# Performance work log

Measured on AMD Instinct MI355X. Metric: run time of the kernel, lower is better.

Reference implementation:

```python
import jax, jax.numpy as jnp
import numpy as np

THETA = 10000.0
NUM_HEADS = 16


def apply_rope(x, pos, theta):
    # x: [..., s, d_k] with d_k even; pos: [s] (broadcasts over leading dims)
    d_k = x.shape[-1]
    inv_freq = 1.0 / (theta ** (jnp.arange(0, d_k, 2, dtype=x.dtype) / d_k))  # [d_k/2]
    ang = pos.astype(x.dtype)[..., None] * inv_freq  # [s, d_k/2]
    cos, sin = jnp.cos(ang), jnp.sin(ang)
    xr = x.reshape(x.shape[:-1] + (d_k // 2, 2))
    x0, x1 = xr[..., 0], xr[..., 1]
    out0 = x0 * cos - x1 * sin
    out1 = x0 * sin + x1 * cos
    return jnp.stack((out0, out1), axis=-1).reshape(x.shape)


def setup_inputs() -> dict:
    key = jax.random.key(0)
    ks = jax.random.split(key, 5)
    B, S, D = 4, 2048, 1024
    sigma = 2.0 / (D + D) ** 0.5
    return {
        "x": jax.random.normal(ks[0], (B, S, D), dtype=jnp.float32),
        "token_positions": jnp.arange(S, dtype=jnp.int64 if jax.config.jax_enable_x64 else jnp.int32),
        "wq": jax.random.normal(ks[1], (D, D), dtype=jnp.float32) * sigma,
        "wk": jax.random.normal(ks[2], (D, D), dtype=jnp.float32) * sigma,
        "wv": jax.random.normal(ks[3], (D, D), dtype=jnp.float32) * sigma,
        "wo": jax.random.normal(ks[4], (D, D), dtype=jnp.float32) * sigma,
    }


def reference(x, token_positions, wq, wk, wv, wo):
    B, S, D = x.shape
    H = NUM_HEADS
    d_k = D // H

    def proj(w, t):  # weight [out, in], t [..., in]
        return jnp.einsum('oi,bsi->bso', w, t)

    def heads(t):  # [b, s, (h d)] -> [b, h, s, d]
        return t.reshape(B, S, H, d_k).transpose(0, 2, 1, 3)

    Q = heads(proj(wq, x))
    K = heads(proj(wk, x))
    V = heads(proj(wv, x))
    Q = apply_rope(Q, token_positions, THETA)
    K = apply_rope(K, token_positions, THETA)

    scores = jnp.einsum('bhqd,bhkd->bhqk', Q, K) * (d_k ** -0.5)
    causal = jnp.tril(jnp.ones((S, S), dtype=bool))
    scores = jnp.where(causal, scores, -jnp.inf)
    attn = jax.nn.softmax(scores.astype(jnp.float32), axis=-1).astype(scores.dtype)
    out = jnp.einsum('bhqk,bhkd->bhqd', attn, V)
    out = out.transpose(0, 2, 1, 3).reshape(B, S, D)
    return jnp.einsum('oi,bsi->bso', wo, out)
```

## Files before the change

### kernel.cpp

```cpp
#include <hip/hip_runtime.h>
#include <cstdint>
#include <cstddef>

#define Bv 4
#define Sv 2048
#define Hv 16
#define Dv 1024
#define Mv (Bv*Sv)

typedef __attribute__((ext_vector_type(8))) short short8;
typedef __attribute__((ext_vector_type(8))) unsigned short ushort8v;
typedef __attribute__((ext_vector_type(4))) float f32x4;

__device__ inline float bf2f(unsigned short u) {
  union { unsigned int i; float f; } x; x.i = ((unsigned int)u) << 16; return x.f;
}
__device__ inline unsigned short f2bf(float f) {
  union { float f; unsigned int i; } x; x.f = f;
  unsigned int r = x.i + 0x7FFFu + ((x.i >> 16) & 1u);
  return (unsigned short)(r >> 16);
}

typedef __attribute__((address_space(1))) const unsigned short gu16;
typedef __attribute__((address_space(3))) unsigned short lu16;
__device__ inline void gld_lds16(const unsigned short* g, unsigned short* l) {
  __builtin_amdgcn_global_load_lds((gu16*)g, (lu16*)l, 16, 0, 0);
}

__global__ __launch_bounds__(256) void cvt_f32_bf16(const float* __restrict__ src,
                                                    unsigned short* __restrict__ dst, int n4) {
  int i = blockIdx.x * 256 + threadIdx.x;
  if (i >= n4) return;
  float4 v = reinterpret_cast<const float4*>(src)[i];
  ushort4 o;
  o.x = f2bf(v.x); o.y = f2bf(v.y); o.z = f2bf(v.z); o.w = f2bf(v.w);
  reinterpret_cast<ushort4*>(dst)[i] = o;
}

__global__ __launch_bounds__(256) void cvt3_f32_bf16(const float* __restrict__ s0,
                                                     const float* __restrict__ s1,
                                                     const float* __restrict__ s2,
                                                     unsigned short* __restrict__ dst) {
  int i = blockIdx.x * 256 + threadIdx.x;
  int w = i >> 18, off = i & 262143;
  const float* src = (w == 0) ? s0 : (w == 1) ? s1 : s2;
  float4 v = reinterpret_cast<const float4*>(src)[off];
  ushort4 o;
  o.x = f2bf(v.x); o.y = f2bf(v.y); o.z = f2bf(v.z); o.w = f2bf(v.w);
  reinterpret_cast<ushort4*>(dst)[i] = o;
}

__global__ __launch_bounds__(256) void rope_table_k(const int* __restrict__ pos,
                                                    float* __restrict__ tab) {
  int idx = blockIdx.x * 256 + threadIdx.x;
  int s = idx >> 5, i = idx & 31;
  float p = (float)pos[s];
  float a = p * __builtin_exp2f(-0.41524101186092027f * (float)i);
  tab[(s << 6) + i]      = __builtin_cosf(a);
  tab[(s << 6) + 32 + i] = __builtin_sinf(a);
}

__device__ __forceinline__ void xcd_swizzle(int& bm, int& bn) {
  const int nx = gridDim.x;
  const int nwg = nx * gridDim.y;
  int flat = blockIdx.y * nx + blockIdx.x;
  if ((nwg & 7) == 0) {
    int q = nwg >> 3;
    flat = (flat & 7) * q + (flat >> 3);
  }
  bm = (flat / nx) * 128;
  bn = (flat % nx) * 128;
}

__device__ inline void storeC(float* p, float v) { *p = v; }
__device__ inline void storeC(unsigned short* p, float v) { *p = f2bf(v); }

template <typename CT>
__global__ __launch_bounds__(256) void gemm_bt_128(
    const unsigned short* __restrict__ A,
    const unsigned short* __restrict__ B,
    CT* __restrict__ C,
    int M, int N, int K) {
  __shared__ unsigned short As[128 * 32];
  __shared__ unsigned short Bs[128 * 32];
  const int tid = threadIdx.x;
  const int wave = tid >> 6, lane = tid & 63;
  int bm, bn;
  xcd_swizzle(bm, bn);
  const int wr = (wave >> 1) * 64, wc = (wave & 1) * 64;

  f32x4 acc[4][4] = {};

  const int c0 = wave * 2, c1 = c0 + 1;
  const int sr0 = c0 * 16 + (lane >> 2);
  const int sr1 = c1 * 16 + (lane >> 2);
  const int scol = (lane & 3) * 8;

  const unsigned short* gA0 = A + (size_t)(bm + sr0) * K + scol;
  const unsigned short* gA1 = A + (size_t)(bm + sr1) * K + scol;
  const unsigned short* gB0 = B + (size_t)(bn + sr0) * K + scol;
  const unsigned short* gB1 = B + (size_t)(bn + sr1) * K + scol;
  unsigned short* lA0 = &As[c0 * 512];
  unsigned short* lA1 = &As[c1 * 512];
  unsigned short* lB0 = &Bs[c0 * 512];
  unsigned short* lB1 = &Bs[c1 * 512];

  const int fr = lane & 15;
  const int fk = (lane >> 4) * 8;

  for (int k0 = 0; k0 < K; k0 += 32) {
    gld_lds16(gA0 + k0, lA0);
    gld_lds16(gA1 + k0, lA1);
    gld_lds16(gB0 + k0, lB0);
    gld_lds16(gB1 + k0, lB1);
    __syncthreads();
    short8 af[4], bfr[4];
#pragma unroll
    for (int m = 0; m < 4; m++)
      af[m] = *reinterpret_cast<const short8*>(&As[(wr + m * 16 + fr) * 32 + fk]);
#pragma unroll
    for (int n = 0; n < 4; n++)
      bfr[n] = *reinterpret_cast<const short8*>(&Bs[(wc + n * 16 + fr) * 32 + fk]);
#pragma unroll
    for (int m = 0; m < 4; m++)
#pragma unroll
      for (int n = 0; n < 4; n++)
        acc[m][n] = __builtin_amdgcn_mfma_f32_16x16x32_bf16(af[m], bfr[n], acc[m][n], 0, 0, 0);
    __syncthreads();
  }

  const int er = (lane >> 4) * 4, ec = lane & 15;
#pragma unroll
  for (int m = 0; m < 4; m++)
#pragma unroll
    for (int n = 0; n < 4; n++)
#pragma unroll
      for (int r = 0; r < 4; r++) {
        int row = bm + wr + m * 16 + er + r;
        int col = bn + wc + n * 16 + ec;
        storeC(&C[(size_t)row * N + col], acc[m][n][r]);
      }
}

__global__ __launch_bounds__(256) void gemm_qkv(
    const unsigned short* __restrict__ A,
    const unsigned short* __restrict__ B,
    unsigned short* __restrict__ Qp,
    unsigned short* __restrict__ Kp,
    unsigned short* __restrict__ Vt,
    const float* __restrict__ tab) {
  const int K = Dv;
  __shared__ unsigned short As[128 * 32];
  __shared__ unsigned short Bs[128 * 32];
  const int tid = threadIdx.x;
  const int wave = tid >> 6, lane = tid & 63;
  int bm, bn;
  xcd_swizzle(bm, bn);
  const int wr = (wave >> 1) * 64, wc = (wave & 1) * 64;

  f32x4 acc[4][4] = {};

  const int c0 = wave * 2, c1 = c0 + 1;
  const int sr0 = c0 * 16 + (lane >> 2);
  const int sr1 = c1 * 16 + (lane >> 2);
  const int scol = (lane & 3) * 8;

  const unsigned short* gA0 = A + (size_t)(bm + sr0) * K + scol;
  const unsigned short* gA1 = A + (size_t)(bm + sr1) * K + scol;
  const unsigned short* gB0 = B + (size_t)(bn + sr0) * K + scol;
  const unsigned short* gB1 = B + (size_t)(bn + sr1) * K + scol;
  unsigned short* lA0 = &As[c0 * 512];
  unsigned short* lA1 = &As[c1 * 512];
  unsigned short* lB0 = &Bs[c0 * 512];
  unsigned short* lB1 = &Bs[c1 * 512];

  const int fr = lane & 15;
  const int fk = (lane >> 4) * 8;

  for (int k0 = 0; k0 < K; k0 += 32) {
    gld_lds16(gA0 + k0, lA0);
    gld_lds16(gA1 + k0, lA1);
    gld_lds16(gB0 + k0, lB0);
    gld_lds16(gB1 + k0, lB1);
    __syncthreads();
    short8 af[4], bfr[4];
#pragma unroll
    for (int m = 0; m < 4; m++)
      af[m] = *reinterpret_cast<const short8*>(&As[(wr + m * 16 + fr) * 32 + fk]);
#pragma unroll
    for (int n = 0; n < 4; n++)
      bfr[n] = *reinterpret_cast<const short8*>(&Bs[(wc + n * 16 + fr) * 32 + fk]);
#pragma unroll
    for (int m = 0; m < 4; m++)
#pragma unroll
      for (int n = 0; n < 4; n++)
        acc[m][n] = __builtin_amdgcn_mfma_f32_16x16x32_bf16(af[m], bfr[n], acc[m][n], 0, 0, 0);
    __syncthreads();
  }

  const int er = (lane >> 4) * 4, ec = lane & 15;
  const int region = bn >> 10;
  if (region < 2) {
    unsigned short* T = (region == 0) ? Qp : Kp;
#pragma unroll
    for (int m = 0; m < 4; m++)
#pragma unroll
      for (int n = 0; n < 4; n++) {
        const int col = bn + wc + n * 16 + ec;
        const int ccol = col & (Dv - 1);
        const int ii = (ccol & 63) >> 1;
        const bool odd = col & 1;
#pragma unroll
        for (int r = 0; r < 4; r++) {
          int row = bm + wr + m * 16 + er + r;
          int s = row & (Sv - 1);
          float v = acc[m][n][r];
          float pv = __shfl_xor(v, 1);
          float cc = tab[(s << 6) + ii];
          float sn = tab[(s << 6) + 32 + ii];
          float o = odd ? __builtin_fmaf(pv, sn, v * cc)
                        : __builtin_fmaf(v, cc, -(pv * sn));
          T[(size_t)row * Dv + ccol] = f2bf(o);
        }
      }
  } else {
#pragma unroll
    for (int m = 0; m < 4; m++)
#pragma unroll
      for (int n = 0; n < 4; n++) {
        const int dfull = (bn - 2048) + wc + n * 16 + ec;
        const int row0 = bm + wr + m * 16 + er;
        const int bb = row0 >> 11, s = row0 & (Sv - 1);
        const size_t vtrow = ((size_t)bb * 16 + (dfull >> 6)) * 64 + (dfull & 63);
        ushort4 ov;
        ov.x = f2bf(acc[m][n][0]);
        ov.y = f2bf(acc[m][n][1]);
        ov.z = f2bf(acc[m][n][2]);
        ov.w = f2bf(acc[m][n][3]);
        *reinterpret_cast<ushort4*>(Vt + vtrow * Sv + s) = ov;
      }
  }
}

__device__ __forceinline__ void softmax_strip(
    f32x4 (&sacc)[2][4], const bool lastt, const int qrel0,
    float (&mrun2)[2], float (&lrun)[2], f32x4 (&oacc)[2][4],
    unsigned int (&pk)[2][4][2]) {
  const float c1 = 0.18033688011112042f;
#pragma unroll
  for (int qf = 0; qf < 2; ++qf) {
    const int qrel = qrel0 + qf * 16;
    float pv[4][4];
    float mx = -INFINITY;
#pragma unroll
    for (int kf = 0; kf < 4; ++kf)
#pragma unroll
      for (int r = 0; r < 4; ++r) {
        float s = sacc[qf][kf][r];
        if (lastt) s = (kf * 16 + r > qrel) ? -INFINITY : s;
        pv[kf][r] = s;
        mx = fmaxf(mx, s);
      }
    mx = fmaxf(mx, __shfl_xor(mx, 16));
    mx = fmaxf(mx, __shfl_xor(mx, 32));
    float pm = mx * c1;
    if (__any(pm > mrun2[qf] + 8.0f)) {
      float m2 = fmaxf(mrun2[qf], pm);
      float sfq = __builtin_exp2f(mrun2[qf] - m2);
      lrun[qf] *= sfq;
#pragma unroll
      for (int dc = 0; dc < 4; ++dc)
#pragma unroll
        for (int r = 0; r < 4; ++r) oacc[qf][dc][r] *= sfq;
      mrun2[qf] = m2;
    }
    const float nm = -mrun2[qf];
    float ps = 0.f;
#pragma unroll
    for (int kf = 0; kf < 4; ++kf)
#pragma unroll
      for (int r = 0; r < 4; ++r) {
        float p = __builtin_exp2f(__builtin_fmaf(pv[kf][r], c1, nm));
        ps += p;
        pv[kf][r] = p;
      }
    ps += __shfl_xor(ps, 16);
    ps += __shfl_xor(ps, 32);
    lrun[qf] += ps;
#pragma unroll
    for (int kf = 0; kf < 4; ++kf)
#pragma unroll
      for (int hh = 0; hh < 2; ++hh) {
        unsigned int rr;
        asm("v_cvt_pk_bf16_f32 %0, %1, %2"
            : "=v"(rr) : "v"(pv[kf][2 * hh]), "v"(pv[kf][2 * hh + 1]));
        pk[qf][kf][hh] = rr;
      }
  }
}

__device__ __forceinline__ void pv_strip(
    const short8 (&vfr)[2][4], const unsigned int (&pk)[2][4][2],
    f32x4 (&oacc)[2][4], const int idx0, const int idx1, const bool hi) {
#pragma unroll
  for (int ks = 0; ks < 2; ++ks)
#pragma unroll
    for (int qf = 0; qf < 2; ++qf) {
      int ra = __builtin_amdgcn_ds_bpermute(idx0, (int)pk[qf][2 * ks][0]);
      int rb = __builtin_amdgcn_ds_bpermute(idx0, (int)pk[qf][2 * ks + 1][0]);
      int rc = __builtin_amdgcn_ds_bpermute(idx0, (int)pk[qf][2 * ks][1]);
      int rd = __builtin_amdgcn_ds_bpermute(idx0, (int)pk[qf][2 * ks + 1][1]);
      int re = __builtin_amdgcn_ds_bpermute(idx1, (int)pk[qf][2 * ks][0]);
      int rf = __builtin_amdgcn_ds_bpermute(idx1, (int)pk[qf][2 * ks + 1][0]);
      int rg = __builtin_amdgcn_ds_bpermute(idx1, (int)pk[qf][2 * ks][1]);
      int rh = __builtin_amdgcn_ds_bpermute(idx1, (int)pk[qf][2 * ks + 1][1]);
      union { unsigned int u[4]; short8 v; } pw;
      pw.u[0] = hi ? (unsigned)rb : (unsigned)ra;
      pw.u[1] = hi ? (unsigned)rd : (unsigned)rc;
      pw.u[2] = hi ? (unsigned)rf : (unsigned)re;
      pw.u[3] = hi ? (unsigned)rh : (unsigned)rg;
      __builtin_amdgcn_s_setprio(1);
#pragma unroll
      for (int dc = 0; dc < 4; ++dc)
        oacc[qf][dc] = __builtin_amdgcn_mfma_f32_16x16x32_bf16(vfr[ks][dc], pw.v, oacc[qf][dc], 0, 0, 0);
      __builtin_amdgcn_s_setprio(0);
    }
}

__global__ __launch_bounds__(256, 2) void attn_mfma(
    const unsigned short* __restrict__ Q,
    const unsigned short* __restrict__ K,
    const unsigned short* __restrict__ Vt,
    unsigned short* __restrict__ O) {
  __shared__ __align__(16) unsigned short ldsK[2][4096];
  __shared__ __align__(16) unsigned short ldsV[2][4096];
  const int tid = threadIdx.x;
  const int wave = tid >> 6, lane = tid & 63;
  const int g = lane >> 4, m = lane & 15;
  const int F = blockIdx.x;
  const int q7 = F >> 3;
  const int bh = ((F & 7) << 3) | (q7 & 7);
  const int bi = q7 >> 3;
  const int b = bh >> 4, h = bh & 15;
  const int j = bi * 4 + wave;
  const int sA = j, sB = 63 - j;
  const int qA0 = sA * 32, qB0 = sB * 32;
  const int ntA = (sA >> 1) + 1, ntB = (sB >> 1) + 1;
  const int ntBmax = ((63 - bi * 4) >> 1) + 1;
  const size_t qkbase = ((size_t)b * Sv) * Dv + (size_t)h * 64;
  const size_t vtbase = (size_t)bh * 64 * Sv;
  const f32x4 zf = {0.f, 0.f, 0.f, 0.f};

  int srowS[2], scolS[2];
#pragma unroll
  for (int i = 0; i < 2; ++i) {
    int s = ((i * 4 + wave) << 6) + lane;
    int s2 = s ^ ((s >> 3) & 7);
    srowS[i] = s2 >> 3;
    scolS[i] = (s2 & 7) * 8;
  }

  short8 qA[2][2], qB[2][2];
#pragma unroll
  for (int qf = 0; qf < 2; ++qf)
#pragma unroll
    for (int ks = 0; ks < 2; ++ks) {
      qA[qf][ks] = *reinterpret_cast<const short8*>(
          Q + qkbase + (size_t)(qA0 + qf * 16 + m) * Dv + ks * 32 + g * 8);
      qB[qf][ks] = *reinterpret_cast<const short8*>(
          Q + qkbase + (size_t)(qB0 + qf * 16 + m) * Dv + ks * 32 + g * 8);
    }

  int offL[2][4];
#pragma unroll
  for (int ks = 0; ks < 2; ++ks)
#pragma unroll
    for (int f = 0; f < 4; ++f)
      offL[ks][f] = (f * 16 + m) * 64 + ((((ks << 2) + g) ^ (m & 7)) * 8);

  f32x4 oA[2][4] = {}, oB[2][4] = {};
  float mA[2] = {-INFINITY, -INFINITY}, mB[2] = {-INFINITY, -INFINITY};
  float lA[2] = {0.f, 0.f}, lB[2] = {0.f, 0.f};

  const int idx0 = (((g & 1) << 5) + m) << 2;
  const int idx1 = idx0 + 64;
  const bool hi = (g >= 2);
  int qrelA = qA0 + m - 4 * g;
  int qrelB = qB0 + m - 4 * g;

  auto STAGE = [&](int c, int t) {
    const int kb = t << 6;
#pragma unroll
    for (int i = 0; i < 2; ++i) {
      gld_lds16(K + qkbase + (size_t)(kb + srowS[i]) * Dv + scolS[i],
                &ldsK[c][(i * 4 + wave) * 512]);
      gld_lds16(Vt + vtbase + (size_t)srowS[i] * Sv + kb + scolS[i],
                &ldsV[c][(i * 4 + wave) * 512]);
    }
  };

  STAGE(0, 0);
  __syncthreads();
  int cur = 0;

  for (int t = 0; t < ntBmax; ++t) {
    if (t + 1 < ntBmax) STAGE(cur ^ 1, t + 1);

    if (t < ntB) {
      const bool actA = (t < ntA);
      f32x4 sAacc[2][4], sBacc[2][4];
      short8 kfr[4];
#pragma unroll
      for (int kf = 0; kf < 4; ++kf)
        kfr[kf] = *reinterpret_cast<const short8*>(&ldsK[cur][offL[0][kf]]);
      __builtin_amdgcn_s_setprio(1);
#pragma unroll
      for (int qf = 0; qf < 2; ++qf)
#pragma unroll
        for (int kf = 0; kf < 4; ++kf)
          sBacc[qf][kf] = __builtin_amdgcn_mfma_f32_16x16x32_bf16(kfr[kf], qB[qf][0], zf, 0, 0, 0);
      if (actA)
#pragma unroll
        for (int qf = 0; qf < 2; ++qf)
#pragma unroll
          for (int kf = 0; kf < 4; ++kf)
            sAacc[qf][kf] = __builtin_amdgcn_mfma_f32_16x16x32_bf16(kfr[kf], qA[qf][0], zf, 0, 0, 0);
      __builtin_amdgcn_s_setprio(0);
#pragma unroll
      for (int kf = 0; kf < 4; ++kf)
        kfr[kf] = *reinterpret_cast<const short8*>(&ldsK[cur][offL[1][kf]]);
      __builtin_amdgcn_s_setprio(1);
#pragma unroll
      for (int qf = 0; qf < 2; ++qf)
#pragma unroll
        for (int kf = 0; kf < 4; ++kf)
          sBacc[qf][kf] = __builtin_amdgcn_mfma_f32_16x16x32_bf16(kfr[kf], qB[qf][1], sBacc[qf][kf], 0, 0, 0);
      if (actA)
#pragma unroll
        for (int qf = 0; qf < 2; ++qf)
#pragma unroll
          for (int kf = 0; kf < 4; ++kf)
            sAacc[qf][kf] = __builtin_amdgcn_mfma_f32_16x16x32_bf16(kfr[kf], qA[qf][1], sAacc[qf][kf], 0, 0, 0);
      __builtin_amdgcn_s_setprio(0);

      short8 vfr[2][4];
#pragma unroll
      for (int ks = 0; ks < 2; ++ks)
#pragma unroll
        for (int dc = 0; dc < 4; ++dc)
          vfr[ks][dc] = *reinterpret_cast<const short8*>(&ldsV[cur][offL[ks][dc]]);

      unsigned int pkB[2][4][2], pkA[2][4][2];
      softmax_strip(sBacc, t == ntB - 1, qrelB, mB, lB, oB, pkB);
      if (actA) softmax_strip(sAacc, t == ntA - 1, qrelA, mA, lA, oA, pkA);
      pv_strip(vfr, pkB, oB, idx0, idx1, hi);
      if (actA) pv_strip(vfr, pkA, oA, idx0, idx1, hi);

      qrelA -= 64; qrelB -= 64;
    }

    __syncthreads();
    cur ^= 1;
  }

#pragma unroll
  for (int qf = 0; qf < 2; ++qf) {
    float rnA = 1.0f / lA[qf];
    float rnB = 1.0f / lB[qf];
    size_t rowA = (size_t)(qA0 + qf * 16 + m);
    size_t rowB = (size_t)(qB0 + qf * 16 + m);
#pragma unroll
    for (int dc = 0; dc < 4; ++dc) {
      ushort4 ov;
      ov.x = f2bf(oA[qf][dc][0] * rnA);
      ov.y = f2bf(oA[qf][dc][1] * rnA);
      ov.z = f2bf(oA[qf][dc][2] * rnA);
      ov.w = f2bf(oA[qf][dc][3] * rnA);
      *reinterpret_cast<ushort4*>(O + qkbase + rowA * Dv + dc * 16 + 4 * g) = ov;
      ov.x = f2bf(oB[qf][dc][0] * rnB);
      ov.y = f2bf(oB[qf][dc][1] * rnB);
      ov.z = f2bf(oB[qf][dc][2] * rnB);
      ov.w = f2bf(oB[qf][dc][3] * rnB);
      *reinterpret_cast<ushort4*>(O + qkbase + rowB * Dv + dc * 16 + 4 * g) = ov;
    }
  }
}

extern "C" void kernel_launch(void* const* d_in, const int* in_sizes, int n_in,
                              void* d_out, int out_size, void* d_ws, size_t ws_size,
                              hipStream_t stream) {
  const float* x   = (const float*)d_in[0];
  const int*   pos = (const int*)d_in[1];
  const float* wq  = (const float*)d_in[2];
  const float* wk  = (const float*)d_in[3];
  const float* wv  = (const float*)d_in[4];
  const float* wo  = (const float*)d_in[5];
  float* out = (float*)d_out;

  char* w = (char*)d_ws;
  unsigned short* xb    = (unsigned short*)(w);
  unsigned short* wqkvb = (unsigned short*)(w + (16u << 20));
  unsigned short* wob   = (unsigned short*)(w + (22u << 20));
  unsigned short* Qp    = (unsigned short*)(w + (24u << 20));
  unsigned short* Kp    = (unsigned short*)(w + (40u << 20));
  unsigned short* Vt    = (unsigned short*)(w + (56u << 20));
  float*          tab   = (float*)(w + (72u << 20));

  rope_table_k<<<(Sv * 32) / 256, 256, 0, stream>>>(pos, tab);
  cvt_f32_bf16<<<(Mv * Dv / 4) / 256, 256, 0, stream>>>(x, xb, Mv * Dv / 4);
  cvt3_f32_bf16<<<(3 * Dv * Dv / 4) / 256, 256, 0, stream>>>(wq, wk, wv, wqkvb);
  cvt_f32_bf16<<<(Dv * Dv / 4) / 256, 256, 0, stream>>>(wo, wob, Dv * Dv / 4);

  gemm_qkv<<<dim3(3 * Dv / 128, Mv / 128), 256, 0, stream>>>(xb, wqkvb, Qp, Kp, Vt, tab);

  attn_mfma<<<512, 256, 0, stream>>>(Qp, Kp, Vt, xb);

  gemm_bt_128<float><<<dim3(Dv / 128, Mv / 128), 256, 0, stream>>>(xb, wob, out, Mv, Dv, Dv);
}
```

Measured before the change: 225.2 us.

## Split attention KV range across wave pairs and merge partial softmax via LDS

Each block now handles two query strip pairs, and each pair is processed by two waves that each cover half of the key range. The waves combine their partial max, sum and output through LDS with a log-sum-exp merge. K and V fragments are now read directly from global memory instead of being staged through double-buffered LDS, and the grid doubles to 1024 blocks. The goal is more parallelism and shorter per-wave serial chains. The cost is that shared K/V reuse across waves is lost, fragment loads become uncoalesced global reads, and a merge step is added.

```diff
diff --git a/kernel.cpp b/kernel.cpp
--- a/kernel.cpp
+++ b/kernel.cpp
@@ -332,33 +332,27 @@
     const unsigned short* __restrict__ K,
     const unsigned short* __restrict__ Vt,
     unsigned short* __restrict__ O) {
-  __shared__ __align__(16) unsigned short ldsK[2][4096];
-  __shared__ __align__(16) unsigned short ldsV[2][4096];
+  __shared__ float cbO[2][64][32];
+  __shared__ float cbML[2][64][4];
   const int tid = threadIdx.x;
   const int wave = tid >> 6, lane = tid & 63;
   const int g = lane >> 4, m = lane & 15;
   const int F = blockIdx.x;
-  const int q7 = F >> 3;
-  const int bh = ((F & 7) << 3) | (q7 & 7);
-  const int bi = q7 >> 3;
-  const int b = bh >> 4, h = bh & 15;
-  const int j = bi * 4 + wave;
+  const int i6 = F >> 3;
+  const int bh = ((F & 7) << 3) | (i6 & 7);
+  const int gidx = i6 >> 3;
+  const int pi = wave >> 1, half = wave & 1;
+  const int j = gidx * 2 + pi;
   const int sA = j, sB = 63 - j;
   const int qA0 = sA * 32, qB0 = sB * 32;
   const int ntA = (sA >> 1) + 1, ntB = (sB >> 1) + 1;
-  const int ntBmax = ((63 - bi * 4) >> 1) + 1;
+  const int T0 = (ntB + 1) >> 1;
+  const int tBeg = half ? T0 : 0;
+  const int tEnd = half ? ntB : T0;
+  const int b = bh >> 4, h = bh & 15;
   const size_t qkbase = ((size_t)b * Sv) * Dv + (size_t)h * 64;
   const size_t vtbase = (size_t)bh * 64 * Sv;
   const f32x4 zf = {0.f, 0.f, 0.f, 0.f};
-
-  int srowS[2], scolS[2];
-#pragma unroll
-  for (int i = 0; i < 2; ++i) {
-    int s = ((i * 4 + wave) << 6) + lane;
-    int s2 = s ^ ((s >> 3) & 7);
-    srowS[i] = s2 >> 3;
-    scolS[i] = (s2 & 7) * 8;
-  }
 
   short8 qA[2][2], qB[2][2];
 #pragma unroll
@@ -371,12 +365,14 @@
           Q + qkbase + (size_t)(qB0 + qf * 16 + m) * Dv + ks * 32 + g * 8);
     }
 
-  int offL[2][4];
-#pragma unroll
-  for (int ks = 0; ks < 2; ++ks)
-#pragma unroll
-    for (int f = 0; f < 4; ++f)
-      offL[ks][f] = (f * 16 + m) * 64 + ((((ks << 2) + g) ^ (m & 7)) * 8);
+  const unsigned short* kp[4];
+  const unsigned short* vp[4];
+#pragma unroll
+  for (int kf = 0; kf < 4; ++kf)
+    kp[kf] = K + qkbase + (size_t)(kf * 16 + m) * Dv + g * 8 + (size_t)tBeg * 64 * Dv;
+#pragma unroll
+  for (int dc = 0; dc < 4; ++dc)
+    vp[dc] = Vt + vtbase + (size_t)(dc * 16 + m) * Sv + g * 8 + tBeg * 64;
 
   f32x4 oA[2][4] = {}, oB[2][4] = {};
   float mA[2] = {-INFINITY, -INFINITY}, mB[2] = {-INFINITY, -INFINITY};
@@ -385,103 +381,143 @@
   const int idx0 = (((g & 1) << 5) + m) << 2;
   const int idx1 = idx0 + 64;
   const bool hi = (g >= 2);
-  int qrelA = qA0 + m - 4 * g;
-  int qrelB = qB0 + m - 4 * g;
-
-  auto STAGE = [&](int c, int t) {
-    const int kb = t << 6;
-#pragma unroll
-    for (int i = 0; i < 2; ++i) {
-      gld_lds16(K + qkbase + (size_t)(kb + srowS[i]) * Dv + scolS[i],
-                &ldsK[c][(i * 4 + wave) * 512]);
-      gld_lds16(Vt + vtbase + (size_t)srowS[i] * Sv + kb + scolS[i],
-                &ldsV[c][(i * 4 + wave) * 512]);
-    }
-  };
-
-  STAGE(0, 0);
+  int qrelA = qA0 + m - 4 * g - tBeg * 64;
+  int qrelB = qB0 + m - 4 * g - tBeg * 64;
+
+  for (int t = tBeg; t < tEnd; ++t) {
+    const bool actA = (t < ntA);
+    f32x4 sAacc[2][4], sBacc[2][4];
+    short8 kfr[4];
+#pragma unroll
+    for (int kf = 0; kf < 4; ++kf)
+      kfr[kf] = *reinterpret_cast<const short8*>(kp[kf]);
+    __builtin_amdgcn_s_setprio(1);
+#pragma unroll
+    for (int qf = 0; qf < 2; ++qf)
+#pragma unroll
+      for (int kf = 0; kf < 4; ++kf)
+        sBacc[qf][kf] = __builtin_amdgcn_mfma_f32_16x16x32_bf16(kfr[kf], qB[qf][0], zf, 0, 0, 0);
+    if (actA)
+#pragma unroll
+      for (int qf = 0; qf < 2; ++qf)
+#pragma unroll
+        for (int kf = 0; kf < 4; ++kf)
+          sAacc[qf][kf] = __builtin_amdgcn_mfma_f32_16x16x32_bf16(kfr[kf], qA[qf][0], zf, 0, 0, 0);
+    __builtin_amdgcn_s_setprio(0);
+#pragma unroll
+    for (int kf = 0; kf < 4; ++kf)
+      kfr[kf] = *reinterpret_cast<const short8*>(kp[kf] + 32);
+    __builtin_amdgcn_s_setprio(1);
+#pragma unroll
+    for (int qf = 0; qf < 2; ++qf)
+#pragma unroll
+      for (int kf = 0; kf < 4; ++kf)
+        sBacc[qf][kf] = __builtin_amdgcn_mfma_f32_16x16x32_bf16(kfr[kf], qB[qf][1], sBacc[qf][kf], 0, 0, 0);
+    if (actA)
+#pragma unroll
+      for (int qf = 0; qf < 2; ++qf)
+#pragma unroll
+        for (int kf = 0; kf < 4; ++kf)
+          sAacc[qf][kf] = __builtin_amdgcn_mfma_f32_16x16x32_bf16(kfr[kf], qA[qf][1], sAacc[qf][kf], 0, 0, 0);
+    __builtin_amdgcn_s_setprio(0);
+
+    short8 vfr[2][4];
+#pragma unroll
+    for (int ks = 0; ks < 2; ++ks)
+#pragma unroll
+      for (int dc = 0; dc < 4; ++dc)
+        vfr[ks][dc] = *reinterpret_cast<const short8*>(vp[dc] + ks * 32);
+
+    unsigned int pkB[2][4][2], pkA[2][4][2];
+    softmax_strip(sBacc, t == ntB - 1, qrelB, mB, lB, oB, pkB);
+    if (actA) softmax_strip(sAacc, t == ntA - 1, qrelA, mA, lA, oA, pkA);
+    pv_strip(vfr, pkB, oB, idx0, idx1, hi);
+    if (actA) pv_strip(vfr, pkA, oA, idx0, idx1, hi);
+
+#pragma unroll
+    for (int kf = 0; kf < 4; ++kf) kp[kf] += (size_t)64 * Dv;
+#pragma unroll
+    for (int dc = 0; dc < 4; ++dc) vp[dc] += 64;
+    qrelA -= 64; qrelB -= 64;
+  }
+
+  if (half) {
+#pragma unroll
+    for (int qf = 0; qf < 2; ++qf) {
+      cbML[pi][lane][qf * 2]     = mB[qf];
+      cbML[pi][lane][qf * 2 + 1] = lB[qf];
+#pragma unroll
+      for (int dc = 0; dc < 4; ++dc)
+#pragma unroll
+        for (int r = 0; r < 4; ++r)
+          cbO[pi][lane][qf * 16 + dc * 4 + r] = oB[qf][dc][r];
+    }
+  }
   __syncthreads();
-  int cur = 0;
-
-  for (int t = 0; t < ntBmax; ++t) {
-    if (t + 1 < ntBmax) STAGE(cur ^ 1, t + 1);
-
-    if (t < ntB) {
-      const bool actA = (t < ntA);
-      f32x4 sAacc[2][4], sBacc[2][4];
-      short8 kfr[4];
-#pragma unroll
-      for (int kf = 0; kf < 4; ++kf)
-        kfr[kf] = *reinterpret_cast<const short8*>(&ldsK[cur][offL[0][kf]]);
-      __builtin_amdgcn_s_setprio(1);
-#pragma unroll
-      for (int qf = 0; qf < 2; ++qf)
-#pragma unroll
-        for (int kf = 0; kf < 4; ++kf)
-          sBacc[qf][kf] = __builtin_amdgcn_mfma_f32_16x16x32_bf16(kfr[kf], qB[qf][0], zf, 0, 0, 0);
-      if (actA)
-#pragma unroll
-        for (int qf = 0; qf < 2; ++qf)
-#pragma unroll
-          for (int kf = 0; kf < 4; ++kf)
-            sAacc[qf][kf] = __builtin_amdgcn_mfma_f32_16x16x32_bf16(kfr[kf], qA[qf][0], zf, 0, 0, 0);
-      __builtin_amdgcn_s_setprio(0);
-#pragma unroll
-      for (int kf = 0; kf < 4; ++kf)
-        kfr[kf] = *reinterpret_cast<const short8*>(&ldsK[cur][offL[1][kf]]);
-      __builtin_amdgcn_s_setprio(1);
-#pragma unroll
-      for (int qf = 0; qf < 2; ++qf)
-#pragma unroll
-        for (int kf = 0; kf < 4; ++kf)
-          sBacc[qf][kf] = __builtin_amdgcn_mfma_f32_16x16x32_bf16(kfr[kf], qB[qf][1], sBacc[qf][kf], 0, 0, 0);
-      if (actA)
-#pragma unroll
-        for (int qf = 0; qf < 2; ++qf)
-#pragma unroll
-          for (int kf = 0; kf < 4; ++kf)
-            sAacc[qf][kf] = __builtin_amdgcn_mfma_f32_16x16x32_bf16(kfr[kf], qA[qf][1], sAacc[qf][kf], 0, 0, 0);
-      __builtin_amdgcn_s_setprio(0);
-
-      short8 vfr[2][4];
-#pragma unroll
-      for (int ks = 0; ks < 2; ++ks)
-#pragma unroll
-        for (int dc = 0; dc < 4; ++dc)
-          vfr[ks][dc] = *reinterpret_cast<const short8*>(&ldsV[cur][offL[ks][dc]]);
-
-      unsigned int pkB[2][4][2], pkA[2][4][2];
-      softmax_strip(sBacc, t == ntB - 1, qrelB, mB, lB, oB, pkB);
-      if (actA) softmax_strip(sAacc, t == ntA - 1, qrelA, mA, lA, oA, pkA);
-      pv_strip(vfr, pkB, oB, idx0, idx1, hi);
-      if (actA) pv_strip(vfr, pkA, oA, idx0, idx1, hi);
-
-      qrelA -= 64; qrelB -= 64;
-    }
-
-    __syncthreads();
-    cur ^= 1;
-  }
-
-#pragma unroll
-  for (int qf = 0; qf < 2; ++qf) {
-    float rnA = 1.0f / lA[qf];
-    float rnB = 1.0f / lB[qf];
-    size_t rowA = (size_t)(qA0 + qf * 16 + m);
-    size_t rowB = (size_t)(qB0 + qf * 16 + m);
-#pragma unroll
-    for (int dc = 0; dc < 4; ++dc) {
-      ushort4 ov;
-      ov.x = f2bf(oA[qf][dc][0] * rnA);
-      ov.y = f2bf(oA[qf][dc][1] * rnA);
-      ov.z = f2bf(oA[qf][dc][2] * rnA);
-      ov.w = f2bf(oA[qf][dc][3] * rnA);
-      *reinterpret_cast<ushort4*>(O + qkbase + rowA * Dv + dc * 16 + 4 * g) = ov;
-      ov.x = f2bf(oB[qf][dc][0] * rnB);
-      ov.y = f2bf(oB[qf][dc][1] * rnB);
-      ov.z = f2bf(oB[qf][dc][2] * rnB);
-      ov.w = f2bf(oB[qf][dc][3] * rnB);
-      *reinterpret_cast<ushort4*>(O + qkbase + rowB * Dv + dc * 16 + 4 * g) = ov;
+  if (!half) {
+#pragma unroll
+    for (int qf = 0; qf < 2; ++qf) {
+      float mH = cbML[pi][lane][qf * 2], lH = cbML[pi][lane][qf * 2 + 1];
+      float m2 = fmaxf(mB[qf], mH);
+      float sfL = __builtin_exp2f(mB[qf] - m2);
+      float sfH = __builtin_exp2f(mH - m2);
+      lB[qf] = lB[qf] * sfL + lH * sfH;
+#pragma unroll
+      for (int dc = 0; dc < 4; ++dc)
+#pragma unroll
+        for (int r = 0; r < 4; ++r)
+          oB[qf][dc][r] = oB[qf][dc][r] * sfL + cbO[pi][lane][qf * 16 + dc * 4 + r] * sfH;
+    }
+  }
+  __syncthreads();
+  if (half) {
+#pragma unroll
+    for (int qf = 0; qf < 2; ++qf) {
+      cbML[pi][lane][qf * 2]     = mA[qf];
+      cbML[pi][lane][qf * 2 + 1] = lA[qf];
+#pragma unroll
+      for (int dc = 0; dc < 4; ++dc)
+#pragma unroll
+        for (int r = 0; r < 4; ++r)
+          cbO[pi][lane][qf * 16 + dc * 4 + r] = oA[qf][dc][r];
+    }
+  }
+  __syncthreads();
+  if (!half) {
+#pragma unroll
+    for (int qf = 0; qf < 2; ++qf) {
+      float mH = cbML[pi][lane][qf * 2], lH = cbML[pi][lane][qf * 2 + 1];
+      float m2 = fmaxf(mA[qf], mH);
+      float sfL = __builtin_exp2f(mA[qf] - m2);
+      float sfH = __builtin_exp2f(mH - m2);
+      lA[qf] = lA[qf] * sfL + lH * sfH;
+#pragma unroll
+      for (int dc = 0; dc < 4; ++dc)
+#pragma unroll
+        for (int r = 0; r < 4; ++r)
+          oA[qf][dc][r] = oA[qf][dc][r] * sfL + cbO[pi][lane][qf * 16 + dc * 4 + r] * sfH;
+    }
+
+#pragma unroll
+    for (int qf = 0; qf < 2; ++qf) {
+      float rnA = 1.0f / lA[qf];
+      float rnB = 1.0f / lB[qf];
+      size_t rowA = (size_t)(qA0 + qf * 16 + m);
+      size_t rowB = (size_t)(qB0 + qf * 16 + m);
+#pragma unroll
+      for (int dc = 0; dc < 4; ++dc) {
+        ushort4 ov;
+        ov.x = f2bf(oA[qf][dc][0] * rnA);
+        ov.y = f2bf(oA[qf][dc][1] * rnA);
+        ov.z = f2bf(oA[qf][dc][2] * rnA);
+        ov.w = f2bf(oA[qf][dc][3] * rnA);
+        *reinterpret_cast<ushort4*>(O + qkbase + rowA * Dv + dc * 16 + 4 * g) = ov;
+        ov.x = f2bf(oB[qf][dc][0] * rnB);
+        ov.y = f2bf(oB[qf][dc][1] * rnB);
+        ov.z = f2bf(oB[qf][dc][2] * rnB);
+        ov.w = f2bf(oB[qf][dc][3] * rnB);
+        *reinterpret_cast<ushort4*>(O + qkbase + rowB * Dv + dc * 16 + 4 * g) = ov;
+      }
     }
   }
 }
@@ -513,7 +549,7 @@
 
   gemm_qkv<<<dim3(3 * Dv / 128, Mv / 128), 256, 0, stream>>>(xb, wqkvb, Qp, Kp, Vt, tab);
 
-  attn_mfma<<<512, 256, 0, stream>>>(Qp, Kp, Vt, xb);
+  attn_mfma<<<1024, 256, 0, stream>>>(Qp, Kp, Vt, xb);
 
   gemm_bt_128<float><<<dim3(Dv / 128, Mv / 128), 256, 0, stream>>>(xb, wob, out, Mv, Dv, Dv);
 }
```

After: 245.9 us. 9.2% more time.

## Triple-buffer attention K/V staging and fuse prep kernels into one launch

Applied to the files above, without the earlier changes.

The attention kernel moves from double to triple LDS buffering. Loads are issued two tiles ahead, with an explicit vmcnt wait and a single barrier per iteration in place of two __syncthreads, so more global-to-LDS latency can be hidden. The four conversion and rope-table kernels are merged into one launch to cut launch overhead. The cost is 50% more LDS in the attention kernel, which could lower occupancy, and correctness now depends on the hand-written vmcnt count.

```diff
diff --git a/kernel.cpp b/kernel.cpp
--- a/kernel.cpp
+++ b/kernel.cpp
@@ -27,37 +27,41 @@
   __builtin_amdgcn_global_load_lds((gu16*)g, (lu16*)l, 16, 0, 0);
 }
 
-__global__ __launch_bounds__(256) void cvt_f32_bf16(const float* __restrict__ src,
-                                                    unsigned short* __restrict__ dst, int n4) {
-  int i = blockIdx.x * 256 + threadIdx.x;
-  if (i >= n4) return;
-  float4 v = reinterpret_cast<const float4*>(src)[i];
-  ushort4 o;
-  o.x = f2bf(v.x); o.y = f2bf(v.y); o.z = f2bf(v.z); o.w = f2bf(v.w);
-  reinterpret_cast<ushort4*>(dst)[i] = o;
-}
-
-__global__ __launch_bounds__(256) void cvt3_f32_bf16(const float* __restrict__ s0,
-                                                     const float* __restrict__ s1,
-                                                     const float* __restrict__ s2,
-                                                     unsigned short* __restrict__ dst) {
-  int i = blockIdx.x * 256 + threadIdx.x;
-  int w = i >> 18, off = i & 262143;
-  const float* src = (w == 0) ? s0 : (w == 1) ? s1 : s2;
-  float4 v = reinterpret_cast<const float4*>(src)[off];
-  ushort4 o;
-  o.x = f2bf(v.x); o.y = f2bf(v.y); o.z = f2bf(v.z); o.w = f2bf(v.w);
-  reinterpret_cast<ushort4*>(dst)[i] = o;
-}
-
-__global__ __launch_bounds__(256) void rope_table_k(const int* __restrict__ pos,
-                                                    float* __restrict__ tab) {
-  int idx = blockIdx.x * 256 + threadIdx.x;
-  int s = idx >> 5, i = idx & 31;
-  float p = (float)pos[s];
-  float a = p * __builtin_exp2f(-0.41524101186092027f * (float)i);
-  tab[(s << 6) + i]      = __builtin_cosf(a);
-  tab[(s << 6) + 32 + i] = __builtin_sinf(a);
+__global__ __launch_bounds__(256) void prep_all(
+    const float* __restrict__ x, const float* __restrict__ wq,
+    const float* __restrict__ wk, const float* __restrict__ wv,
+    const float* __restrict__ wo, const int* __restrict__ pos,
+    unsigned short* __restrict__ xb, unsigned short* __restrict__ wqkvb,
+    unsigned short* __restrict__ wob, float* __restrict__ tab) {
+  const int bb = blockIdx.x, tid = threadIdx.x;
+  if (bb < 8192) {
+    int i = bb * 256 + tid;
+    float4 v = reinterpret_cast<const float4*>(x)[i];
+    ushort4 o;
+    o.x = f2bf(v.x); o.y = f2bf(v.y); o.z = f2bf(v.z); o.w = f2bf(v.w);
+    reinterpret_cast<ushort4*>(xb)[i] = o;
+  } else if (bb < 11264) {
+    int i = (bb - 8192) * 256 + tid;
+    int w = i >> 18, off = i & 262143;
+    const float* src = (w == 0) ? wq : (w == 1) ? wk : wv;
+    float4 v = reinterpret_cast<const float4*>(src)[off];
+    ushort4 o;
+    o.x = f2bf(v.x); o.y = f2bf(v.y); o.z = f2bf(v.z); o.w = f2bf(v.w);
+    reinterpret_cast<ushort4*>(wqkvb)[i] = o;
+  } else if (bb < 12288) {
+    int i = (bb - 11264) * 256 + tid;
+    float4 v = reinterpret_cast<const float4*>(wo)[i];
+    ushort4 o;
+    o.x = f2bf(v.x); o.y = f2bf(v.y); o.z = f2bf(v.z); o.w = f2bf(v.w);
+    reinterpret_cast<ushort4*>(wob)[i] = o;
+  } else {
+    int idx = (bb - 12288) * 256 + tid;
+    int s = idx >> 5, i = idx & 31;
+    float p = (float)pos[s];
+    float a = p * __builtin_exp2f(-0.41524101186092027f * (float)i);
+    tab[(s << 6) + i]      = __builtin_cosf(a);
+    tab[(s << 6) + 32 + i] = __builtin_sinf(a);
+  }
 }
 
 __device__ __forceinline__ void xcd_swizzle(int& bm, int& bn) {
@@ -332,8 +336,8 @@
     const unsigned short* __restrict__ K,
     const unsigned short* __restrict__ Vt,
     unsigned short* __restrict__ O) {
-  __shared__ __align__(16) unsigned short ldsK[2][4096];
-  __shared__ __align__(16) unsigned short ldsV[2][4096];
+  __shared__ __align__(16) unsigned short ldsK[3][4096];
+  __shared__ __align__(16) unsigned short ldsV[3][4096];
   const int tid = threadIdx.x;
   const int wave = tid >> 6, lane = tid & 63;
   const int g = lane >> 4, m = lane & 15;
@@ -400,11 +404,18 @@
   };
 
   STAGE(0, 0);
-  __syncthreads();
-  int cur = 0;
+  STAGE(1, 1);
+  int cur = 0, bs = 2;
 
   for (int t = 0; t < ntBmax; ++t) {
-    if (t + 1 < ntBmax) STAGE(cur ^ 1, t + 1);
+    if (t + 1 < ntBmax) {
+      asm volatile("s_waitcnt vmcnt(4)" ::: "memory");
+    } else {
+      asm volatile("s_waitcnt vmcnt(0)" ::: "memory");
+    }
+    __builtin_amdgcn_sched_barrier(0);
+    __builtin_amdgcn_s_barrier();
+    if (t + 2 < ntBmax) STAGE(bs, t + 2);
 
     if (t < ntB) {
       const bool actA = (t < ntA);
@@ -459,8 +470,8 @@
       qrelA -= 64; qrelB -= 64;
     }
 
-    __syncthreads();
-    cur ^= 1;
+    cur = (cur == 2) ? 0 : cur + 1;
+    bs = (bs == 2) ? 0 : bs + 1;
   }
 
 #pragma unroll
@@ -506,10 +517,7 @@
   unsigned short* Vt    = (unsigned short*)(w + (56u << 20));
   float*          tab   = (float*)(w + (72u << 20));
 
-  rope_table_k<<<(Sv * 32) / 256, 256, 0, stream>>>(pos, tab);
-  cvt_f32_bf16<<<(Mv * Dv / 4) / 256, 256, 0, stream>>>(x, xb, Mv * Dv / 4);
-  cvt3_f32_bf16<<<(3 * Dv * Dv / 4) / 256, 256, 0, stream>>>(wq, wk, wv, wqkvb);
-  cvt_f32_bf16<<<(Dv * Dv / 4) / 256, 256, 0, stream>>>(wo, wob, Dv * Dv / 4);
+  prep_all<<<12544, 256, 0, stream>>>(x, wq, wk, wv, wo, pos, xb, wqkvb, wob, tab);
 
   gemm_qkv<<<dim3(3 * Dv / 128, Mv / 128), 256, 0, stream>>>(xb, wqkvb, Qp, Kp, Vt, tab);
 
```

Result: faster. 215.9 us (-4.1%).
